# Kernel tuning notes

Hardware: AMD Instinct MI355X
Metric: run time of the kernel (lower is better)

## Reference

```python
import jax, jax.numpy as jnp
import numpy as np

N_HEADS = 8

def setup_inputs() -> dict:
    key = jax.random.key(0)
    ks = jax.random.split(key, 5)
    d = 256
    B, N = 2, 4096
    scale = 1.0 / np.sqrt(d)
    return {
        "x_q": jax.random.normal(ks[0], (B, N, d), jnp.float32),
        "x_kv": jax.random.normal(ks[1], (B, N, d), jnp.float32),
        "Wq": jax.random.normal(ks[2], (d, d), jnp.float32) * scale,
        "bq": jnp.zeros((d,), jnp.float32),
        "Wk": jax.random.normal(ks[3], (d, d), jnp.float32) * scale,
        "bk": jnp.zeros((d,), jnp.float32),
        "Wv": jax.random.normal(ks[4], (d, d), jnp.float32) * scale,
        "bv": jnp.zeros((d,), jnp.float32),
    }


def reference(x_q, x_kv, Wq, bq, Wk, bk, Wv, bv):
    B, Nq, d = x_q.shape
    H = N_HEADS
    dh = d // H
    # linear projections (torch Linear: x @ W^T + b)
    q = x_q @ Wq.T + bq            # [B, Nq, d]
    k = x_kv @ Wk.T + bk           # [B, Nk, d]
    v = x_kv @ Wv.T + bv           # [B, Nk, d]
    # split heads -> [B, H, N, dh]
    q = q.reshape(B, Nq, H, dh).transpose(0, 2, 1, 3)
    k = k.reshape(B, -1, H, dh).transpose(0, 2, 1, 3)
    v = v.reshape(B, -1, H, dh).transpose(0, 2, 1, 3)
    # scores [B, H, Nq, Nk], softmax over keys
    scores = jnp.einsum('bhqd,bhkd->bhqk', q, k) / jnp.sqrt(jnp.asarray(dh, q.dtype))
    attn = jax.nn.softmax(scores, axis=-1)
    out = jnp.einsum('bhqk,bhkd->bhqd', attn, v)   # [B, H, Nq, dh]
    return out.transpose(0, 2, 1, 3).reshape(B, Nq, H * dh)
```

## Files before the change

kernel.cpp:

```cpp
#include <hip/hip_runtime.h>
#include <stdint.h>

#define BATCH 2
#define NSEQ 4096
#define DM 256
#define NHEAD 8
#define DH 32
#define SCALE 0.17677669529663687f
#define QPRE (SCALE * 1.44269504088896340736f)

#if __has_builtin(__builtin_amdgcn_exp2f)
#define EXP2W(x) __builtin_amdgcn_exp2f(x)
#else
#define EXP2W(x) exp2f(x)
#endif

#define WAIT_VM0() asm volatile("s_waitcnt vmcnt(0)" ::: "memory")

typedef unsigned short ushort_t;
typedef __attribute__((ext_vector_type(8))) short short8;
typedef __attribute__((ext_vector_type(4))) float float4v;

__device__ __forceinline__ ushort_t f2bf(float f) {
    union { float f; uint32_t i; } x; x.f = f;
    uint32_t i = x.i;
    i += ((i >> 16) & 1u) + 0x7fffu;
    return (ushort_t)(i >> 16);
}
__device__ __forceinline__ uint32_t rne16(float f) {
    const uint32_t i = __float_as_uint(f);
    return i + 0x7fffu + ((i >> 16) & 1u);
}
#if __has_builtin(__builtin_amdgcn_cvt_pk_bf16_f32)
typedef __bf16 bf16x2_t __attribute__((ext_vector_type(2)));
__device__ __forceinline__ uint32_t pk2(float a, float b) {
    union { bf16x2_t v; uint32_t u; } c;
    c.v = __builtin_amdgcn_cvt_pk_bf16_f32(a, b);
    return c.u;
}
#else
__device__ __forceinline__ uint32_t pk2(float a, float b) {
    return __builtin_amdgcn_perm(rne16(b), rne16(a), 0x07060302u);
}
#endif

__device__ __forceinline__ void load_lds_16B(const void* g, void* lds) {
    __builtin_amdgcn_global_load_lds(
        (const __attribute__((address_space(1))) void*)g,
        (__attribute__((address_space(3))) void*)lds, 16, 0, 0);
}

__global__ __launch_bounds__(256) void packw_kernel(
    const float* __restrict__ Wq, const float* __restrict__ Wk,
    const float* __restrict__ Wv, ushort_t* __restrict__ Wp)
{
    const int mat = blockIdx.x >> 5;
    const int off = (((blockIdx.x & 31) << 8) + threadIdx.x) * 8;
    const float* W = (mat == 0) ? Wq : (mat == 1) ? Wk : Wv;
    const float s  = (mat == 0) ? QPRE : 1.0f;
    float4 a = *(const float4*)(W + off);
    float4 b = *(const float4*)(W + off + 4);
    uint32_t d[4] = { pk2(a.x * s, a.y * s), pk2(a.z * s, a.w * s),
                      pk2(b.x * s, b.y * s), pk2(b.z * s, b.w * s) };
    *(uint4*)(Wp + (size_t)mat * (DM * DM) + off) = *(const uint4*)d;
}

#define RST 264
__global__ __launch_bounds__(256) void proj_kernel(
    const float* __restrict__ x_q, const float* __restrict__ x_kv,
    const ushort_t* __restrict__ Wp,
    const float* __restrict__ bq, const float* __restrict__ bk,
    const float* __restrict__ bv,
    ushort_t* __restrict__ Qh, ushort_t* __restrict__ Kh,
    ushort_t* __restrict__ Vt)
{
    const int mat = blockIdx.y;
    const int n0  = blockIdx.x * 32;
    const float* x    = (mat == 0) ? x_q : x_kv;
    const ushort_t* W = Wp + (size_t)mat * (DM * DM);
    const float* bias = (mat == 0) ? bq : (mat == 1) ? bk : bv;
    const float bscale = (mat == 0) ? QPRE : 1.0f;

    __shared__ __align__(16) ushort_t xls[32 * RST];
    const int t = threadIdx.x;
    {
        const int r  = t >> 3;
        const int c0 = (t & 7) * 32;
        const float* src = x + (size_t)(n0 + r) * DM + c0;
        uint32_t d[16];
        #pragma unroll
        for (int i = 0; i < 8; i++) {
            float4 v = *(const float4*)(src + i * 4);
            d[i * 2]     = pk2(v.x, v.y);
            d[i * 2 + 1] = pk2(v.z, v.w);
        }
        uint32_t* dst = (uint32_t*)&xls[r * RST + c0];
        #pragma unroll
        for (int i = 0; i < 4; i++)
            *(uint4*)(dst + i * 4) = *(const uint4*)&d[i * 4];
    }
    __syncthreads();

    const int w    = t >> 6;
    const int l    = t & 63;
    const int lm   = l & 15;
    const int quad = l >> 4;
    const int j0   = w * 64;

    float4v acc[2][4];
    #pragma unroll
    for (int rt = 0; rt < 2; rt++)
        #pragma unroll
        for (int jt = 0; jt < 4; jt++)
            acc[rt][jt] = (float4v){0.f, 0.f, 0.f, 0.f};

    for (int kc = 0; kc < DM / 32; kc++) {
        short8 af[2];
        #pragma unroll
        for (int rt = 0; rt < 2; rt++)
            af[rt] = *(const short8*)&xls[(rt * 16 + lm) * RST + kc * 32 + quad * 8];
        #pragma unroll
        for (int jt = 0; jt < 4; jt++) {
            short8 bf = *(const short8*)(W + (size_t)(j0 + jt * 16 + lm) * DM
                                           + kc * 32 + quad * 8);
            if (mat == 2) {
                acc[0][jt] = __builtin_amdgcn_mfma_f32_16x16x32_bf16(af[0], bf, acc[0][jt], 0, 0, 0);
                acc[1][jt] = __builtin_amdgcn_mfma_f32_16x16x32_bf16(af[1], bf, acc[1][jt], 0, 0, 0);
            } else {
                acc[0][jt] = __builtin_amdgcn_mfma_f32_16x16x32_bf16(bf, af[0], acc[0][jt], 0, 0, 0);
                acc[1][jt] = __builtin_amdgcn_mfma_f32_16x16x32_bf16(bf, af[1], acc[1][jt], 0, 0, 0);
            }
        }
    }

    const int bb = n0 >> 12;
    const int cn = n0 & (NSEQ - 1);
    if (mat == 2) {
        #pragma unroll
        for (int jt = 0; jt < 4; jt++) {
            const int j  = j0 + jt * 16 + lm;
            const int h  = j >> 5, dd = j & 31;
            const int bh = bb * NHEAD + h;
            const float bj = bias[j];
            #pragma unroll
            for (int rt = 0; rt < 2; rt++) {
                union { ushort_t u[4]; uint2 v; } pk;
                #pragma unroll
                for (int r = 0; r < 4; r++) pk.u[r] = f2bf(acc[rt][jt][r] + bj);
                *(uint2*)&Vt[((size_t)bh * DH + dd) * NSEQ + cn + quad * 8 + rt * 4] = pk.v;
            }
        }
    } else {
        ushort_t* dst = (mat == 0) ? Qh : Kh;
        #pragma unroll
        for (int jt = 0; jt < 4; jt++) {
            const int jb = j0 + jt * 16 + quad * 4;
            const int h  = jb >> 5, dd0 = jb & 31;
            const int bh = bb * NHEAD + h;
            float4 b4 = *(const float4*)(bias + jb);
            #pragma unroll
            for (int rt = 0; rt < 2; rt++) {
                const int n = cn + rt * 16 + lm;
                union { ushort_t u[4]; uint2 v; } pk;
                pk.u[0] = f2bf(acc[rt][jt][0] + b4.x * bscale);
                pk.u[1] = f2bf(acc[rt][jt][1] + b4.y * bscale);
                pk.u[2] = f2bf(acc[rt][jt][2] + b4.z * bscale);
                pk.u[3] = f2bf(acc[rt][jt][3] + b4.w * bscale);
                *(uint2*)&dst[((size_t)bh * NSEQ + n) * DH + dd0] = pk.v;
            }
        }
    }
}

#define QT 2
__global__ __launch_bounds__(256) void fattn_kernel(
    const ushort_t* __restrict__ Qh, const ushort_t* __restrict__ Kh,
    const ushort_t* __restrict__ Vt, float* __restrict__ out)
{
    const int blk  = blockIdx.x;
    const int xcd  = blk & 7;
    const int jj   = blk >> 3;
    const int bh   = xcd * 2 + (jj & 1);
    const int qblk = jj >> 1;
    const int b    = bh >> 3, h = bh & 7;

    const int w    = threadIdx.x >> 6;
    const int l    = threadIdx.x & 63;
    const int lm   = l & 15;
    const int quad = l >> 4;
    const int q0   = qblk * 128 + w * 32;

    __shared__ __align__(16) ushort_t tiles[2][2048];

    const ushort_t* Qb = Qh + (size_t)bh * NSEQ * DH;
    const ushort_t* Kb = Kh + (size_t)bh * NSEQ * DH;
    const ushort_t* Vb = Vt + (size_t)bh * DH * NSEQ;

    const ushort_t* gsrc;
    int gadv;
    if (w < 2) { gsrc = Kb + (size_t)(w * 16 + (l >> 2)) * DH + (l & 3) * 8;  gadv = 32 * DH; }
    else       { gsrc = Vb + (size_t)((w - 2) * 16 + (l >> 2)) * NSEQ + (l & 3) * 8; gadv = 32; }

    short8 qf[QT];
    #pragma unroll
    for (int qt = 0; qt < QT; qt++)
        qf[qt] = *(const short8*)(Qb + (size_t)(q0 + qt * 16 + lm) * DH + quad * 8);

    short8 ones;
    #pragma unroll
    for (int i = 0; i < 8; i++) ones[i] = (short)0x3F80;

    float4v accO[QT][2], accL[QT];
    #pragma unroll
    for (int qt = 0; qt < QT; qt++) {
        accO[qt][0] = (float4v){0.f, 0.f, 0.f, 0.f};
        accO[qt][1] = (float4v){0.f, 0.f, 0.f, 0.f};
        accL[qt]    = (float4v){0.f, 0.f, 0.f, 0.f};
    }
    const float4v zero = {0.f, 0.f, 0.f, 0.f};

    load_lds_16B(gsrc, &tiles[0][w * 512]);
    gsrc += gadv;

    for (int it = 0; it < NSEQ / 32; it++) {
        WAIT_VM0();
        __syncthreads();
        if (it < NSEQ / 32 - 1) {
            load_lds_16B(gsrc, &tiles[(it + 1) & 1][w * 512]);
            gsrc += gadv;
        }

        const ushort_t* Kt = &tiles[it & 1][0];
        const ushort_t* Vl = &tiles[it & 1][1024];
        short8 kf0 = *(const short8*)&Kt[lm * 32 + quad * 8];
        short8 kf1 = *(const short8*)&Kt[512 + lm * 32 + quad * 8];
        short8 vf0 = *(const short8*)&Vl[lm * 32 + quad * 8];
        short8 vf1 = *(const short8*)&Vl[512 + lm * 32 + quad * 8];

        #pragma unroll
        for (int qt = 0; qt < QT; qt++) {
            float4v s0 = __builtin_amdgcn_mfma_f32_16x16x32_bf16(kf0, qf[qt], zero, 0, 0, 0);
            float4v s1 = __builtin_amdgcn_mfma_f32_16x16x32_bf16(kf1, qf[qt], zero, 0, 0, 0);
            float p0[4], p1[4];
            #pragma unroll
            for (int r = 0; r < 4; r++) {
                p0[r] = EXP2W(s0[r]);
                p1[r] = EXP2W(s1[r]);
            }
            uint32_t pd[4] = { pk2(p0[0], p0[1]), pk2(p0[2], p0[3]),
                               pk2(p1[0], p1[1]), pk2(p1[2], p1[3]) };
            short8 pf = *(const short8*)pd;
            accO[qt][0] = __builtin_amdgcn_mfma_f32_16x16x32_bf16(pf, vf0, accO[qt][0], 0, 0, 0);
            accO[qt][1] = __builtin_amdgcn_mfma_f32_16x16x32_bf16(pf, vf1, accO[qt][1], 0, 0, 0);
            accL[qt]    = __builtin_amdgcn_mfma_f32_16x16x32_bf16(pf, ones, accL[qt], 0, 0, 0);
        }
    }

    #pragma unroll
    for (int qt = 0; qt < QT; qt++)
        #pragma unroll
        for (int r = 0; r < 4; r++) {
            const float inv = 1.0f / accL[qt][r];
            const int q = q0 + qt * 16 + quad * 4 + r;
            float* orow = out + ((size_t)b * NSEQ + q) * DM + h * DH;
            orow[lm]      = accO[qt][0][r] * inv;
            orow[16 + lm] = accO[qt][1][r] * inv;
        }
}

#define KITERS 32
__global__ __launch_bounds__(256) void fattn_split_kernel(
    const ushort_t* __restrict__ Qh, const ushort_t* __restrict__ Kh,
    const ushort_t* __restrict__ Vt, float* __restrict__ out,
    float* __restrict__ Opart, float* __restrict__ Lp)
{
    const int blk  = blockIdx.x;
    const int xcd  = blk & 7;
    const int jj   = blk >> 3;
    const int bh   = xcd * 2 + (jj & 1);
    const int qblk = (jj >> 1) & 31;
    const int khalf = jj >> 6;
    const int b    = bh >> 3, h = bh & 7;

    const int w    = threadIdx.x >> 6;
    const int l    = threadIdx.x & 63;
    const int lm   = l & 15;
    const int quad = l >> 4;
    const int q0   = qblk * 128 + w * 32;

    __shared__ __align__(16) ushort_t tiles[2][4096];

    const ushort_t* Qb = Qh + (size_t)bh * NSEQ * DH;
    const ushort_t* Kb = Kh + (size_t)bh * NSEQ * DH + (size_t)khalf * 2048 * DH;
    const ushort_t* Vb = Vt + (size_t)bh * DH * NSEQ + (size_t)khalf * 2048;

    const ushort_t *gsA, *gsB;
    int dA, dB, gadv;
    if (w < 2) {
        gsA  = Kb + (size_t)(w * 32 + (l >> 2)) * DH + (l & 3) * 8;
        gsB  = gsA + 16 * DH;
        dA   = w * 1024;  dB = dA + 512;
        gadv = 64 * DH;
    } else {
        gsA  = Vb + (size_t)(l >> 2) * NSEQ + (w - 2) * 32 + (l & 3) * 8;
        gsB  = gsA + 16 * NSEQ;
        dA   = 2048 + (w - 2) * 1024;  dB = dA + 512;
        gadv = 64;
    }

    short8 qf[QT];
    #pragma unroll
    for (int qt = 0; qt < QT; qt++)
        qf[qt] = *(const short8*)(Qb + (size_t)(q0 + qt * 16 + lm) * DH + quad * 8);

    short8 ones;
    #pragma unroll
    for (int i = 0; i < 8; i++) ones[i] = (short)0x3F80;

    float4v accO[QT][2], accL[QT];
    #pragma unroll
    for (int qt = 0; qt < QT; qt++) {
        accO[qt][0] = (float4v){0.f, 0.f, 0.f, 0.f};
        accO[qt][1] = (float4v){0.f, 0.f, 0.f, 0.f};
        accL[qt]    = (float4v){0.f, 0.f, 0.f, 0.f};
    }
    const float4v zero = {0.f, 0.f, 0.f, 0.f};

    load_lds_16B(gsA, &tiles[0][dA]);
    load_lds_16B(gsB, &tiles[0][dB]);
    gsA += gadv;  gsB += gadv;

    for (int it = 0; it < KITERS; it++) {
        WAIT_VM0();
        __syncthreads();
        if (it < KITERS - 1) {
            load_lds_16B(gsA, &tiles[(it + 1) & 1][dA]);
            load_lds_16B(gsB, &tiles[(it + 1) & 1][dB]);
            gsA += gadv;  gsB += gadv;
        }

        const ushort_t* Kt  = &tiles[it & 1][0];
        const ushort_t* Vla = &tiles[it & 1][2048];
        const ushort_t* Vlb = &tiles[it & 1][3072];
        short8 kf0 = *(const short8*)&Kt[lm * 32 + quad * 8];
        short8 kf1 = *(const short8*)&Kt[512 + lm * 32 + quad * 8];
        short8 kf2 = *(const short8*)&Kt[1024 + lm * 32 + quad * 8];
        short8 kf3 = *(const short8*)&Kt[1536 + lm * 32 + quad * 8];
        short8 va0 = *(const short8*)&Vla[lm * 32 + quad * 8];
        short8 va1 = *(const short8*)&Vla[512 + lm * 32 + quad * 8];
        short8 vb0 = *(const short8*)&Vlb[lm * 32 + quad * 8];
        short8 vb1 = *(const short8*)&Vlb[512 + lm * 32 + quad * 8];

        #pragma unroll
        for (int qt = 0; qt < QT; qt++) {
            float4v s0 = __builtin_amdgcn_mfma_f32_16x16x32_bf16(kf0, qf[qt], zero, 0, 0, 0);
            float4v s1 = __builtin_amdgcn_mfma_f32_16x16x32_bf16(kf1, qf[qt], zero, 0, 0, 0);
            float4v s2 = __builtin_amdgcn_mfma_f32_16x16x32_bf16(kf2, qf[qt], zero, 0, 0, 0);
            float4v s3 = __builtin_amdgcn_mfma_f32_16x16x32_bf16(kf3, qf[qt], zero, 0, 0, 0);
            float p0[4], p1[4], p2[4], p3[4];
            #pragma unroll
            for (int r = 0; r < 4; r++) {
                p0[r] = EXP2W(s0[r]);
                p1[r] = EXP2W(s1[r]);
                p2[r] = EXP2W(s2[r]);
                p3[r] = EXP2W(s3[r]);
            }
            uint32_t pda[4] = { pk2(p0[0], p0[1]), pk2(p0[2], p0[3]),
                                pk2(p1[0], p1[1]), pk2(p1[2], p1[3]) };
            uint32_t pdb[4] = { pk2(p2[0], p2[1]), pk2(p2[2], p2[3]),
                                pk2(p3[0], p3[1]), pk2(p3[2], p3[3]) };
            short8 pfa = *(const short8*)pda;
            short8 pfb = *(const short8*)pdb;
            accO[qt][0] = __builtin_amdgcn_mfma_f32_16x16x32_bf16(pfa, va0, accO[qt][0], 0, 0, 0);
            accO[qt][1] = __builtin_amdgcn_mfma_f32_16x16x32_bf16(pfa, va1, accO[qt][1], 0, 0, 0);
            accL[qt]    = __builtin_amdgcn_mfma_f32_16x16x32_bf16(pfa, ones, accL[qt], 0, 0, 0);
            accO[qt][0] = __builtin_amdgcn_mfma_f32_16x16x32_bf16(pfb, vb0, accO[qt][0], 0, 0, 0);
            accO[qt][1] = __builtin_amdgcn_mfma_f32_16x16x32_bf16(pfb, vb1, accO[qt][1], 0, 0, 0);
            accL[qt]    = __builtin_amdgcn_mfma_f32_16x16x32_bf16(pfb, ones, accL[qt], 0, 0, 0);
        }
    }

    float* Od = (khalf == 0) ? out : Opart;
    #pragma unroll
    for (int qt = 0; qt < QT; qt++)
        #pragma unroll
        for (int r = 0; r < 4; r++) {
            const int q = q0 + qt * 16 + quad * 4 + r;
            float* orow = Od + ((size_t)b * NSEQ + q) * DM + h * DH;
            orow[lm]      = accO[qt][0][r];
            orow[16 + lm] = accO[qt][1][r];
            if (lm == 0)
                Lp[khalf * (16 * NSEQ) + bh * NSEQ + q] = accL[qt][r];
        }
}

__global__ __launch_bounds__(256) void combine_kernel(
    float* __restrict__ out, const float* __restrict__ Opart,
    const float* __restrict__ Lp)
{
    const int t   = blockIdx.x * 256 + threadIdx.x;
    const size_t base = (size_t)t * 8;
    const int b   = (int)(base >> 20);
    const int rem = (int)(base & ((1u << 20) - 1));
    const int q   = rem >> 8;
    const int dm  = rem & 255;
    const int h   = dm >> 5;
    const int bh  = b * NHEAD + h;
    const float l0 = Lp[bh * NSEQ + q];
    const float l1 = Lp[16 * NSEQ + bh * NSEQ + q];
    const float inv = 1.0f / (l0 + l1);
    float4 a0 = *(const float4*)(out + base);
    float4 a1 = *(const float4*)(out + base + 4);
    float4 c0 = *(const float4*)(Opart + base);
    float4 c1 = *(const float4*)(Opart + base + 4);
    a0.x = (a0.x + c0.x) * inv;  a0.y = (a0.y + c0.y) * inv;
    a0.z = (a0.z + c0.z) * inv;  a0.w = (a0.w + c0.w) * inv;
    a1.x = (a1.x + c1.x) * inv;  a1.y = (a1.y + c1.y) * inv;
    a1.z = (a1.z + c1.z) * inv;  a1.w = (a1.w + c1.w) * inv;
    *(float4*)(out + base)     = a0;
    *(float4*)(out + base + 4) = a1;
}

extern "C" void kernel_launch(void* const* d_in, const int* in_sizes, int n_in,
                              void* d_out, int out_size, void* d_ws, size_t ws_size,
                              hipStream_t stream)
{
    const float* x_q  = (const float*)d_in[0];
    const float* x_kv = (const float*)d_in[1];
    const float* Wq   = (const float*)d_in[2];
    const float* bq   = (const float*)d_in[3];
    const float* Wk   = (const float*)d_in[4];
    const float* bk   = (const float*)d_in[5];
    const float* Wv   = (const float*)d_in[6];
    const float* bv   = (const float*)d_in[7];
    float* out = (float*)d_out;

    const size_t per = (size_t)BATCH * NHEAD * NSEQ * DH;
    ushort_t* Qh = (ushort_t*)d_ws;
    ushort_t* Kh = Qh + per;
    ushort_t* Vt = Kh + per;
    ushort_t* Wp = (ushort_t*)d_out;

    const size_t qkv_bytes   = per * 3 * sizeof(ushort_t);
    const size_t opart_elems = (size_t)BATCH * NSEQ * DM;
    const size_t lp_elems    = (size_t)2 * 16 * NSEQ;
    const size_t need = qkv_bytes + (opart_elems + lp_elems) * sizeof(float);
    float* Opart = (float*)((char*)d_ws + qkv_bytes);
    float* Lp    = Opart + opart_elems;

    packw_kernel<<<96, 256, 0, stream>>>(Wq, Wk, Wv, Wp);

    dim3 pgrid(BATCH * NSEQ / 32, 3);
    proj_kernel<<<pgrid, 256, 0, stream>>>(x_q, x_kv, Wp, bq, bk, bv,
                                           Qh, Kh, Vt);

    if (ws_size >= need) {
        fattn_split_kernel<<<1024, 256, 0, stream>>>(Qh, Kh, Vt, out, Opart, Lp);
        combine_kernel<<<(BATCH * NSEQ * DM) / (256 * 8), 256, 0, stream>>>(out, Opart, Lp);
    } else {
        fattn_kernel<<<512, 256, 0, stream>>>(Qh, Kh, Vt, out);
    }
}
```

Baseline: 165.3 us.

## Load K/V fragments directly from global memory instead of staging through LDS

```diff
diff --git a/kernel.cpp b/kernel.cpp
--- a/kernel.cpp
+++ b/kernel.cpp
@@ -288,25 +288,13 @@
     const int quad = l >> 4;
     const int q0   = qblk * 128 + w * 32;
 
-    __shared__ __align__(16) ushort_t tiles[2][4096];
-
     const ushort_t* Qb = Qh + (size_t)bh * NSEQ * DH;
     const ushort_t* Kb = Kh + (size_t)bh * NSEQ * DH + (size_t)khalf * 2048 * DH;
     const ushort_t* Vb = Vt + (size_t)bh * DH * NSEQ + (size_t)khalf * 2048;
 
-    const ushort_t *gsA, *gsB;
-    int dA, dB, gadv;
-    if (w < 2) {
-        gsA  = Kb + (size_t)(w * 32 + (l >> 2)) * DH + (l & 3) * 8;
-        gsB  = gsA + 16 * DH;
-        dA   = w * 1024;  dB = dA + 512;
-        gadv = 64 * DH;
-    } else {
-        gsA  = Vb + (size_t)(l >> 2) * NSEQ + (w - 2) * 32 + (l & 3) * 8;
-        gsB  = gsA + 16 * NSEQ;
-        dA   = 2048 + (w - 2) * 1024;  dB = dA + 512;
-        gadv = 64;
-    }
+    const ushort_t* pK  = Kb + lm * DH + quad * 8;
+    const ushort_t* pV0 = Vb + (size_t)lm * NSEQ + quad * 8;
+    const ushort_t* pV1 = pV0 + (size_t)16 * NSEQ;
 
     short8 qf[QT];
     #pragma unroll
@@ -326,30 +314,16 @@
     }
     const float4v zero = {0.f, 0.f, 0.f, 0.f};
 
-    load_lds_16B(gsA, &tiles[0][dA]);
-    load_lds_16B(gsB, &tiles[0][dB]);
-    gsA += gadv;  gsB += gadv;
-
     for (int it = 0; it < KITERS; it++) {
-        WAIT_VM0();
-        __syncthreads();
-        if (it < KITERS - 1) {
-            load_lds_16B(gsA, &tiles[(it + 1) & 1][dA]);
-            load_lds_16B(gsB, &tiles[(it + 1) & 1][dB]);
-            gsA += gadv;  gsB += gadv;
-        }
-
-        const ushort_t* Kt  = &tiles[it & 1][0];
-        const ushort_t* Vla = &tiles[it & 1][2048];
-        const ushort_t* Vlb = &tiles[it & 1][3072];
-        short8 kf0 = *(const short8*)&Kt[lm * 32 + quad * 8];
-        short8 kf1 = *(const short8*)&Kt[512 + lm * 32 + quad * 8];
-        short8 kf2 = *(const short8*)&Kt[1024 + lm * 32 + quad * 8];
-        short8 kf3 = *(const short8*)&Kt[1536 + lm * 32 + quad * 8];
-        short8 va0 = *(const short8*)&Vla[lm * 32 + quad * 8];
-        short8 va1 = *(const short8*)&Vla[512 + lm * 32 + quad * 8];
-        short8 vb0 = *(const short8*)&Vlb[lm * 32 + quad * 8];
-        short8 vb1 = *(const short8*)&Vlb[512 + lm * 32 + quad * 8];
+        const int ko = it * 64;
+        short8 kf0 = *(const short8*)(pK + (size_t)ko * DH);
+        short8 kf1 = *(const short8*)(pK + (size_t)ko * DH + 16 * DH);
+        short8 kf2 = *(const short8*)(pK + (size_t)ko * DH + 32 * DH);
+        short8 kf3 = *(const short8*)(pK + (size_t)ko * DH + 48 * DH);
+        short8 va0 = *(const short8*)(pV0 + ko);
+        short8 va1 = *(const short8*)(pV1 + ko);
+        short8 vb0 = *(const short8*)(pV0 + ko + 32);
+        short8 vb1 = *(const short8*)(pV1 + ko + 32);
 
         #pragma unroll
         for (int qt = 0; qt < QT; qt++) {
```

After: 190.1 us. 15.0% more time.

## Split attention keys four ways and fold weight packing into projection

Applied to the files above, without the earlier changes.

```diff
diff --git a/kernel.cpp b/kernel.cpp
--- a/kernel.cpp
+++ b/kernel.cpp
@@ -50,25 +50,11 @@
         (__attribute__((address_space(3))) void*)lds, 16, 0, 0);
 }
 
-__global__ __launch_bounds__(256) void packw_kernel(
-    const float* __restrict__ Wq, const float* __restrict__ Wk,
-    const float* __restrict__ Wv, ushort_t* __restrict__ Wp)
-{
-    const int mat = blockIdx.x >> 5;
-    const int off = (((blockIdx.x & 31) << 8) + threadIdx.x) * 8;
-    const float* W = (mat == 0) ? Wq : (mat == 1) ? Wk : Wv;
-    const float s  = (mat == 0) ? QPRE : 1.0f;
-    float4 a = *(const float4*)(W + off);
-    float4 b = *(const float4*)(W + off + 4);
-    uint32_t d[4] = { pk2(a.x * s, a.y * s), pk2(a.z * s, a.w * s),
-                      pk2(b.x * s, b.y * s), pk2(b.z * s, b.w * s) };
-    *(uint4*)(Wp + (size_t)mat * (DM * DM) + off) = *(const uint4*)d;
-}
-
 #define RST 264
 __global__ __launch_bounds__(256) void proj_kernel(
     const float* __restrict__ x_q, const float* __restrict__ x_kv,
-    const ushort_t* __restrict__ Wp,
+    const float* __restrict__ Wq, const float* __restrict__ Wk,
+    const float* __restrict__ Wv,
     const float* __restrict__ bq, const float* __restrict__ bk,
     const float* __restrict__ bv,
     ushort_t* __restrict__ Qh, ushort_t* __restrict__ Kh,
@@ -77,8 +63,9 @@
     const int mat = blockIdx.y;
     const int n0  = blockIdx.x * 32;
     const float* x    = (mat == 0) ? x_q : x_kv;
-    const ushort_t* W = Wp + (size_t)mat * (DM * DM);
+    const float* W    = (mat == 0) ? Wq : (mat == 1) ? Wk : Wv;
     const float* bias = (mat == 0) ? bq : (mat == 1) ? bk : bv;
+    const float ws     = (mat == 0) ? QPRE : 1.0f;
     const float bscale = (mat == 0) ? QPRE : 1.0f;
 
     __shared__ __align__(16) ushort_t xls[32 * RST];
@@ -121,8 +108,12 @@
             af[rt] = *(const short8*)&xls[(rt * 16 + lm) * RST + kc * 32 + quad * 8];
         #pragma unroll
         for (int jt = 0; jt < 4; jt++) {
-            short8 bf = *(const short8*)(W + (size_t)(j0 + jt * 16 + lm) * DM
-                                           + kc * 32 + quad * 8);
+            const float* wsrc = W + (size_t)(j0 + jt * 16 + lm) * DM + kc * 32 + quad * 8;
+            float4 wa = *(const float4*)(wsrc);
+            float4 wb = *(const float4*)(wsrc + 4);
+            uint32_t wd[4] = { pk2(wa.x * ws, wa.y * ws), pk2(wa.z * ws, wa.w * ws),
+                               pk2(wb.x * ws, wb.y * ws), pk2(wb.z * ws, wb.w * ws) };
+            short8 bf = *(const short8*)wd;
             if (mat == 2) {
                 acc[0][jt] = __builtin_amdgcn_mfma_f32_16x16x32_bf16(af[0], bf, acc[0][jt], 0, 0, 0);
                 acc[1][jt] = __builtin_amdgcn_mfma_f32_16x16x32_bf16(af[1], bf, acc[1][jt], 0, 0, 0);
@@ -268,8 +259,9 @@
         }
 }
 
-#define KITERS 32
-__global__ __launch_bounds__(256) void fattn_split_kernel(
+#define KITERS4 16
+#define OPELEMS ((size_t)BATCH * NSEQ * DM)
+__global__ __launch_bounds__(256, 8) void fattn_split4_kernel(
     const ushort_t* __restrict__ Qh, const ushort_t* __restrict__ Kh,
     const ushort_t* __restrict__ Vt, float* __restrict__ out,
     float* __restrict__ Opart, float* __restrict__ Lp)
@@ -279,7 +271,7 @@
     const int jj   = blk >> 3;
     const int bh   = xcd * 2 + (jj & 1);
     const int qblk = (jj >> 1) & 31;
-    const int khalf = jj >> 6;
+    const int kq   = jj >> 6;
     const int b    = bh >> 3, h = bh & 7;
 
     const int w    = threadIdx.x >> 6;
@@ -291,8 +283,8 @@
     __shared__ __align__(16) ushort_t tiles[2][4096];
 
     const ushort_t* Qb = Qh + (size_t)bh * NSEQ * DH;
-    const ushort_t* Kb = Kh + (size_t)bh * NSEQ * DH + (size_t)khalf * 2048 * DH;
-    const ushort_t* Vb = Vt + (size_t)bh * DH * NSEQ + (size_t)khalf * 2048;
+    const ushort_t* Kb = Kh + (size_t)bh * NSEQ * DH + (size_t)kq * 1024 * DH;
+    const ushort_t* Vb = Vt + (size_t)bh * DH * NSEQ + (size_t)kq * 1024;
 
     const ushort_t *gsA, *gsB;
     int dA, dB, gadv;
@@ -330,10 +322,10 @@
     load_lds_16B(gsB, &tiles[0][dB]);
     gsA += gadv;  gsB += gadv;
 
-    for (int it = 0; it < KITERS; it++) {
+    for (int it = 0; it < KITERS4; it++) {
         WAIT_VM0();
         __syncthreads();
-        if (it < KITERS - 1) {
+        if (it < KITERS4 - 1) {
             load_lds_16B(gsA, &tiles[(it + 1) & 1][dA]);
             load_lds_16B(gsB, &tiles[(it + 1) & 1][dB]);
             gsA += gadv;  gsB += gadv;
@@ -380,7 +372,7 @@
         }
     }
 
-    float* Od = (khalf == 0) ? out : Opart;
+    float* Od = (kq == 0) ? out : Opart + (size_t)(kq - 1) * OPELEMS;
     #pragma unroll
     for (int qt = 0; qt < QT; qt++)
         #pragma unroll
@@ -390,11 +382,11 @@
             orow[lm]      = accO[qt][0][r];
             orow[16 + lm] = accO[qt][1][r];
             if (lm == 0)
-                Lp[khalf * (16 * NSEQ) + bh * NSEQ + q] = accL[qt][r];
-        }
-}
-
-__global__ __launch_bounds__(256) void combine_kernel(
+                Lp[kq * (16 * NSEQ) + bh * NSEQ + q] = accL[qt][r];
+        }
+}
+
+__global__ __launch_bounds__(256) void combine4_kernel(
     float* __restrict__ out, const float* __restrict__ Opart,
     const float* __restrict__ Lp)
 {
@@ -406,17 +398,22 @@
     const int dm  = rem & 255;
     const int h   = dm >> 5;
     const int bh  = b * NHEAD + h;
-    const float l0 = Lp[bh * NSEQ + q];
-    const float l1 = Lp[16 * NSEQ + bh * NSEQ + q];
-    const float inv = 1.0f / (l0 + l1);
+    float lsum = 0.f;
+    #pragma unroll
+    for (int kq = 0; kq < 4; kq++)
+        lsum += Lp[kq * (16 * NSEQ) + bh * NSEQ + q];
+    const float inv = 1.0f / lsum;
     float4 a0 = *(const float4*)(out + base);
     float4 a1 = *(const float4*)(out + base + 4);
-    float4 c0 = *(const float4*)(Opart + base);
-    float4 c1 = *(const float4*)(Opart + base + 4);
-    a0.x = (a0.x + c0.x) * inv;  a0.y = (a0.y + c0.y) * inv;
-    a0.z = (a0.z + c0.z) * inv;  a0.w = (a0.w + c0.w) * inv;
-    a1.x = (a1.x + c1.x) * inv;  a1.y = (a1.y + c1.y) * inv;
-    a1.z = (a1.z + c1.z) * inv;  a1.w = (a1.w + c1.w) * inv;
+    #pragma unroll
+    for (int p = 0; p < 3; p++) {
+        float4 c0 = *(const float4*)(Opart + p * OPELEMS + base);
+        float4 c1 = *(const float4*)(Opart + p * OPELEMS + base + 4);
+        a0.x += c0.x;  a0.y += c0.y;  a0.z += c0.z;  a0.w += c0.w;
+        a1.x += c1.x;  a1.y += c1.y;  a1.z += c1.z;  a1.w += c1.w;
+    }
+    a0.x *= inv;  a0.y *= inv;  a0.z *= inv;  a0.w *= inv;
+    a1.x *= inv;  a1.y *= inv;  a1.z *= inv;  a1.w *= inv;
     *(float4*)(out + base)     = a0;
     *(float4*)(out + base + 4) = a1;
 }
@@ -439,24 +436,20 @@
     ushort_t* Qh = (ushort_t*)d_ws;
     ushort_t* Kh = Qh + per;
     ushort_t* Vt = Kh + per;
-    ushort_t* Wp = (ushort_t*)d_out;
-
-    const size_t qkv_bytes   = per * 3 * sizeof(ushort_t);
-    const size_t opart_elems = (size_t)BATCH * NSEQ * DM;
-    const size_t lp_elems    = (size_t)2 * 16 * NSEQ;
-    const size_t need = qkv_bytes + (opart_elems + lp_elems) * sizeof(float);
+
+    const size_t qkv_bytes = per * 3 * sizeof(ushort_t);
+    const size_t lp_elems  = (size_t)4 * 16 * NSEQ;
+    const size_t need4 = qkv_bytes + (3 * OPELEMS + lp_elems) * sizeof(float);
     float* Opart = (float*)((char*)d_ws + qkv_bytes);
-    float* Lp    = Opart + opart_elems;
-
-    packw_kernel<<<96, 256, 0, stream>>>(Wq, Wk, Wv, Wp);
+    float* Lp    = Opart + 3 * OPELEMS;
 
     dim3 pgrid(BATCH * NSEQ / 32, 3);
-    proj_kernel<<<pgrid, 256, 0, stream>>>(x_q, x_kv, Wp, bq, bk, bv,
+    proj_kernel<<<pgrid, 256, 0, stream>>>(x_q, x_kv, Wq, Wk, Wv, bq, bk, bv,
                                            Qh, Kh, Vt);
 
-    if (ws_size >= need) {
-        fattn_split_kernel<<<1024, 256, 0, stream>>>(Qh, Kh, Vt, out, Opart, Lp);
-        combine_kernel<<<(BATCH * NSEQ * DM) / (256 * 8), 256, 0, stream>>>(out, Opart, Lp);
+    if (ws_size >= need4) {
+        fattn_split4_kernel<<<2048, 256, 0, stream>>>(Qh, Kh, Vt, out, Opart, Lp);
+        combine4_kernel<<<(BATCH * NSEQ * DM) / (256 * 8), 256, 0, stream>>>(out, Opart, Lp);
     } else {
         fattn_kernel<<<512, 256, 0, stream>>>(Qh, Kh, Vt, out);
     }
```

After: 178.6 us. +8.0%, slower.
